# Kernel optimization log

Hardware: AMD Instinct MI355X
Metric: run time of the kernel (lower is better)

## Reference

```python
import jax, jax.numpy as jnp
import numpy as np

SEQ, BATCH, HIDDEN = 4096, 16, 512

def setup_inputs() -> dict:
    key = jax.random.key(0)
    kf, kx, kh = jax.random.split(key, 3)
    f = jax.random.uniform(kf, (SEQ, BATCH, HIDDEN), dtype=jnp.float32)
    x = jax.random.normal(kx, (SEQ, BATCH, HIDDEN), dtype=jnp.float32)
    hidden_init = jax.random.normal(kh, (BATCH, HIDDEN), dtype=jnp.float32)
    return {"f": f, "x": x, "hidden_init": hidden_init}

def reference(f, x, hidden_init):
    # h_t = f_t * x_t + (1 - f_t) * h_{t-1}
    # Linear recurrence h_t = a_t * h_{t-1} + b_t with a = 1-f, b = f*x.
    # Solved with an associative scan: compose (a1,b1) then (a2,b2) ->
    # (a1*a2, a2*b1 + b2). After the scan, A_t = prod(a_1..a_t) and
    # B_t = h_t assuming h_0 = 0, so h_t = B_t + A_t * h_init.
    a = 1.0 - f                      # (S, B, H)
    b = f * x                        # (S, B, H)

    def combine(c1, c2):
        a1, b1 = c1
        a2, b2 = c2
        return (a1 * a2, a2 * b1 + b2)

    A, B = jax.lax.associative_scan(combine, (a, b), axis=0)
    return B + A * hidden_init[None, :, :]
```

## Files before the change

kernel.cpp:

```cpp
#include <hip/hip_runtime.h>


#define SQ      4096
#define NC4     2048
#define NCH     8192
#define TT      16
#define NCHUNK  (SQ / TT)
#define GRID1   (NCHUNK * 8)

typedef float floatx4 __attribute__((ext_vector_type(4)));

__global__ __launch_bounds__(256, 2)
void fm_agg(const floatx4* __restrict__ f4, const floatx4* __restrict__ x4,
            floatx4* __restrict__ aggA, floatx4* __restrict__ aggB)
{
  const int tid   = threadIdx.x;
  const int chunk = blockIdx.x >> 3;
  const int col   = ((blockIdx.x & 7) << 8) + tid;
  const size_t base = (size_t)(chunk * TT) * NC4 + col;

  floatx4 ff[TT], xx[TT];
#pragma unroll
  for (int t = 0; t < TT; ++t) {
    ff[t] = f4[base + (size_t)t * NC4];
    xx[t] = x4[base + (size_t)t * NC4];
  }
  __builtin_amdgcn_sched_barrier(0);

  floatx4 A = {1.f, 1.f, 1.f, 1.f};
  floatx4 B = {0.f, 0.f, 0.f, 0.f};
#pragma unroll
  for (int t = 0; t < TT; ++t) {
    B.x = fmaf(ff[t].x, xx[t].x - B.x, B.x);
    B.y = fmaf(ff[t].y, xx[t].y - B.y, B.y);
    B.z = fmaf(ff[t].z, xx[t].z - B.z, B.z);
    B.w = fmaf(ff[t].w, xx[t].w - B.w, B.w);
    A.x = fmaf(-ff[t].x, A.x, A.x);
    A.y = fmaf(-ff[t].y, A.y, A.y);
    A.z = fmaf(-ff[t].z, A.z, A.z);
    A.w = fmaf(-ff[t].w, A.w, A.w);
  }
  aggA[(size_t)chunk * NC4 + col] = A;
  aggB[(size_t)chunk * NC4 + col] = B;
}

__global__ __launch_bounds__(256, 4)
void fm_mid(const float* __restrict__ A, float* __restrict__ B,
            const float* __restrict__ h0)
{
  const int chain = blockIdx.x * 256 + threadIdx.x;
  float h = h0[chain];
  for (int cb = 0; cb < NCHUNK / 16; ++cb) {
    float a[16], b[16];
#pragma unroll
    for (int i = 0; i < 16; ++i) {
      const size_t idx = (size_t)(cb * 16 + i) * NCH + chain;
      a[i] = A[idx];
      b[i] = B[idx];
    }
#pragma unroll
    for (int i = 0; i < 16; ++i) {
      const size_t idx = (size_t)(cb * 16 + i) * NCH + chain;
      B[idx] = h;
      h = fmaf(a[i], h, b[i]);
    }
  }
}

__global__ __launch_bounds__(256, 2)
void fm_apply(const floatx4* __restrict__ f4, const floatx4* __restrict__ x4,
              const floatx4* __restrict__ hprev4, floatx4* __restrict__ out4)
{
  const int tid   = threadIdx.x;
  const int chunk = (NCHUNK - 1) - (blockIdx.x >> 3);
  const int col   = ((blockIdx.x & 7) << 8) + tid;
  const size_t base = (size_t)(chunk * TT) * NC4 + col;

  floatx4 ff[TT], xx[TT];
#pragma unroll
  for (int t = 0; t < TT; ++t) {
    ff[t] = f4[base + (size_t)t * NC4];
    xx[t] = x4[base + (size_t)t * NC4];
  }
  floatx4 h = hprev4[(size_t)chunk * NC4 + col];
  __builtin_amdgcn_sched_barrier(0);

#pragma unroll
  for (int t = 0; t < TT; ++t) {
    h.x = fmaf(ff[t].x, xx[t].x - h.x, h.x);
    h.y = fmaf(ff[t].y, xx[t].y - h.y, h.y);
    h.z = fmaf(ff[t].z, xx[t].z - h.z, h.z);
    h.w = fmaf(ff[t].w, xx[t].w - h.w, h.w);
    __builtin_nontemporal_store(h, &out4[base + (size_t)t * NC4]);
  }
}

__global__ void fm_naive(const float4* __restrict__ f4, const float4* __restrict__ x4,
                         const float4* __restrict__ h04, float4* __restrict__ out4)
{
  const int col = blockIdx.x * blockDim.x + threadIdx.x;
  if (col >= NC4) return;
  float4 h = h04[col];
  for (int t = 0; t < SQ; ++t) {
    const size_t idx = (size_t)t * NC4 + col;
    const float4 ff = f4[idx], xx = x4[idx];
    h.x = fmaf(ff.x, xx.x - h.x, h.x);
    h.y = fmaf(ff.y, xx.y - h.y, h.y);
    h.z = fmaf(ff.z, xx.z - h.z, h.z);
    h.w = fmaf(ff.w, xx.w - h.w, h.w);
    out4[idx] = h;
  }
}

extern "C" void kernel_launch(void* const* d_in, const int* in_sizes, int n_in,
                              void* d_out, int out_size, void* d_ws, size_t ws_size,
                              hipStream_t stream)
{
  const floatx4* f4  = (const floatx4*)d_in[0];
  const floatx4* x4  = (const floatx4*)d_in[1];
  const float*   h0  = (const float*)d_in[2];
  floatx4* out4 = (floatx4*)d_out;

  const size_t AGG = (size_t)NCHUNK * NC4 * 16;

  if (ws_size >= 2 * AGG) {
    floatx4* aggA = (floatx4*)d_ws;
    floatx4* aggB = (floatx4*)((char*)d_ws + AGG);
    fm_agg<<<GRID1, 256, 0, stream>>>(f4, x4, aggA, aggB);
    fm_mid<<<NCH / 256, 256, 0, stream>>>((const float*)aggA,
                                          (float*)aggB, h0);
    fm_apply<<<GRID1, 256, 0, stream>>>(f4, x4, (const floatx4*)aggB, out4);
  } else {
    fm_naive<<<(NC4 + 255) / 256, 256, 0, stream>>>((const float4*)f4,
                                                    (const float4*)x4,
                                                    (const float4*)h0,
                                                    (float4*)out4);
  }
}
```

Baseline: 371.0 us.

## Fuse three-pass scan into one cooperative kernel with grid barriers

Replaces the three separate launches (chunk aggregate, serial chunk-carry, apply) with a single cooperative kernel of 256 blocks that uses software grid barriers between phases. The middle carry pass is parallelised into a two-level scan over 16 segments, so the long serial chain over 256 chunks becomes short chains. Chunk length doubles to 32 and the fallback kernels stream loads instead of register-buffering them. This removes launch gaps and the single-chain latency bottleneck, at the cost of a barrier memset, spin-wait synchronisation and a dependence on cooperative-launch support and co-residency.

```diff
diff --git a/kernel.cpp b/kernel.cpp
--- a/kernel.cpp
+++ b/kernel.cpp
@@ -4,41 +4,171 @@
 #define SQ      4096
 #define NC4     2048
 #define NCH     8192
-#define TT      16
+#define TT      32
 #define NCHUNK  (SQ / TT)
-#define GRID1   (NCHUNK * 8)
+#define NBLK    256
+#define SEGS    16
+#define CPS     (NCHUNK / SEGS)
+
+#define AGGA_OFF  0u
+#define AGGB_OFF  4194304u
+#define SEGA_OFF  8388608u
+#define SEGB_OFF  8912896u
+#define SEGH_OFF  9437184u
+#define BAR_OFF   9961472u
+#define WS_NEED   (BAR_OFF + 2048u)
 
 typedef float floatx4 __attribute__((ext_vector_type(4)));
 
-__global__ __launch_bounds__(256, 2)
+#define FM_B(B,F,X) \
+  B.x = fmaf(F.x, X.x - B.x, B.x); B.y = fmaf(F.y, X.y - B.y, B.y); \
+  B.z = fmaf(F.z, X.z - B.z, B.z); B.w = fmaf(F.w, X.w - B.w, B.w);
+#define FM_A(A,F) \
+  A.x = fmaf(-F.x, A.x, A.x); A.y = fmaf(-F.y, A.y, A.y); \
+  A.z = fmaf(-F.z, A.z, A.z); A.w = fmaf(-F.w, A.w, A.w);
+
+__device__ __forceinline__ void grid_barrier(unsigned* bar, int gen)
+{
+  __syncthreads();
+  if (threadIdx.x == 0) {
+    __threadfence();
+    __hip_atomic_fetch_add(&bar[(gen * 8 + (blockIdx.x & 7)) * 16], 1u,
+                           __ATOMIC_RELEASE, __HIP_MEMORY_SCOPE_AGENT);
+    unsigned sum;
+    do {
+      sum = 0;
+#pragma unroll
+      for (int s = 0; s < 8; ++s)
+        sum += __hip_atomic_load(&bar[(gen * 8 + s) * 16],
+                                 __ATOMIC_RELAXED, __HIP_MEMORY_SCOPE_AGENT);
+      if (sum < (unsigned)NBLK) __builtin_amdgcn_s_sleep(8);
+    } while (sum < (unsigned)NBLK);
+    __threadfence();
+  }
+  __syncthreads();
+}
+
+__global__ __launch_bounds__(512, 2)
+void fm_fused(const floatx4* __restrict__ f4, const floatx4* __restrict__ x4,
+              const float* __restrict__ h0, char* __restrict__ ws,
+              floatx4* __restrict__ out4)
+{
+  floatx4*  aggA4 = (floatx4*)(ws + AGGA_OFF);
+  floatx4*  aggB4 = (floatx4*)(ws + AGGB_OFF);
+  float*    aggAs = (float*)(ws + AGGA_OFF);
+  float*    aggBs = (float*)(ws + AGGB_OFF);
+  float*    segA  = (float*)(ws + SEGA_OFF);
+  float*    segB  = (float*)(ws + SEGB_OFF);
+  float*    segH  = (float*)(ws + SEGH_OFF);
+  unsigned* bar   = (unsigned*)(ws + BAR_OFF);
+
+  const int bid = blockIdx.x, tid = threadIdx.x;
+  const int chunk = bid >> 1;
+  const int c0 = ((bid & 1) << 10) + tid;
+  const int c1 = c0 + 512;
+  const size_t tbase = (size_t)chunk * TT * NC4;
+
+  {
+    floatx4 A0 = {1.f,1.f,1.f,1.f}, A1 = {1.f,1.f,1.f,1.f};
+    floatx4 B0 = {0.f,0.f,0.f,0.f}, B1 = {0.f,0.f,0.f,0.f};
+#pragma unroll 8
+    for (int t = 0; t < TT; ++t) {
+      const size_t r = tbase + (size_t)t * NC4;
+      const floatx4 F0 = f4[r + c0], X0 = x4[r + c0];
+      const floatx4 F1 = f4[r + c1], X1 = x4[r + c1];
+      FM_B(B0, F0, X0)  FM_A(A0, F0)
+      FM_B(B1, F1, X1)  FM_A(A1, F1)
+    }
+    aggA4[(size_t)chunk * NC4 + c0] = A0;
+    aggA4[(size_t)chunk * NC4 + c1] = A1;
+    aggB4[(size_t)chunk * NC4 + c0] = B0;
+    aggB4[(size_t)chunk * NC4 + c1] = B1;
+  }
+  grid_barrier(bar, 0);
+
+  {
+    const int g = bid * 512 + tid;
+    const int chain = g & (NCH - 1);
+    const int seg   = g >> 13;
+    float a = 1.f, b = 0.f;
+#pragma unroll
+    for (int i = 0; i < CPS; ++i) {
+      const size_t idx = (size_t)(seg * CPS + i) * NCH + chain;
+      const float ac = aggAs[idx], bc = aggBs[idx];
+      b = fmaf(ac, b, bc);
+      a *= ac;
+    }
+    segA[seg * NCH + chain] = a;
+    segB[seg * NCH + chain] = b;
+  }
+  grid_barrier(bar, 1);
+
+  if (bid < 16) {
+    const int chain = bid * 512 + tid;
+    float h = h0[chain];
+#pragma unroll
+    for (int s = 0; s < SEGS; ++s) {
+      segH[s * NCH + chain] = h;
+      h = fmaf(segA[s * NCH + chain], h, segB[s * NCH + chain]);
+    }
+  }
+  grid_barrier(bar, 2);
+
+  {
+    const int g = bid * 512 + tid;
+    const int chain = g & (NCH - 1);
+    const int seg   = g >> 13;
+    float h = segH[seg * NCH + chain];
+    float a[CPS], b[CPS];
+#pragma unroll
+    for (int i = 0; i < CPS; ++i) {
+      const size_t idx = (size_t)(seg * CPS + i) * NCH + chain;
+      a[i] = aggAs[idx];
+      b[i] = aggBs[idx];
+    }
+#pragma unroll
+    for (int i = 0; i < CPS; ++i) {
+      const size_t idx = (size_t)(seg * CPS + i) * NCH + chain;
+      aggBs[idx] = h;
+      h = fmaf(a[i], h, b[i]);
+    }
+  }
+  grid_barrier(bar, 3);
+
+  {
+    floatx4 H0 = aggB4[(size_t)chunk * NC4 + c0];
+    floatx4 H1 = aggB4[(size_t)chunk * NC4 + c1];
+#pragma unroll 8
+    for (int t = 0; t < TT; ++t) {
+      const size_t r = tbase + (size_t)t * NC4;
+      const floatx4 F0 = f4[r + c0], X0 = x4[r + c0];
+      const floatx4 F1 = f4[r + c1], X1 = x4[r + c1];
+      FM_B(H0, F0, X0)
+      FM_B(H1, F1, X1)
+      __builtin_nontemporal_store(H0, &out4[r + c0]);
+      __builtin_nontemporal_store(H1, &out4[r + c1]);
+    }
+  }
+}
+
+#define FTT     16
+#define FNCHUNK (SQ / FTT)
+
+__global__ __launch_bounds__(256, 4)
 void fm_agg(const floatx4* __restrict__ f4, const floatx4* __restrict__ x4,
             floatx4* __restrict__ aggA, floatx4* __restrict__ aggB)
 {
   const int tid   = threadIdx.x;
   const int chunk = blockIdx.x >> 3;
   const int col   = ((blockIdx.x & 7) << 8) + tid;
-  const size_t base = (size_t)(chunk * TT) * NC4 + col;
-
-  floatx4 ff[TT], xx[TT];
-#pragma unroll
-  for (int t = 0; t < TT; ++t) {
-    ff[t] = f4[base + (size_t)t * NC4];
-    xx[t] = x4[base + (size_t)t * NC4];
-  }
-  __builtin_amdgcn_sched_barrier(0);
-
-  floatx4 A = {1.f, 1.f, 1.f, 1.f};
-  floatx4 B = {0.f, 0.f, 0.f, 0.f};
-#pragma unroll
-  for (int t = 0; t < TT; ++t) {
-    B.x = fmaf(ff[t].x, xx[t].x - B.x, B.x);
-    B.y = fmaf(ff[t].y, xx[t].y - B.y, B.y);
-    B.z = fmaf(ff[t].z, xx[t].z - B.z, B.z);
-    B.w = fmaf(ff[t].w, xx[t].w - B.w, B.w);
-    A.x = fmaf(-ff[t].x, A.x, A.x);
-    A.y = fmaf(-ff[t].y, A.y, A.y);
-    A.z = fmaf(-ff[t].z, A.z, A.z);
-    A.w = fmaf(-ff[t].w, A.w, A.w);
+  const size_t base = (size_t)(chunk * FTT) * NC4 + col;
+
+  floatx4 A = {1.f,1.f,1.f,1.f}, B = {0.f,0.f,0.f,0.f};
+#pragma unroll 8
+  for (int t = 0; t < FTT; ++t) {
+    const floatx4 F = f4[base + (size_t)t * NC4];
+    const floatx4 X = x4[base + (size_t)t * NC4];
+    FM_B(B, F, X)  FM_A(A, F)
   }
   aggA[(size_t)chunk * NC4 + col] = A;
   aggB[(size_t)chunk * NC4 + col] = B;
@@ -50,7 +180,7 @@
 {
   const int chain = blockIdx.x * 256 + threadIdx.x;
   float h = h0[chain];
-  for (int cb = 0; cb < NCHUNK / 16; ++cb) {
+  for (int cb = 0; cb < FNCHUNK / 16; ++cb) {
     float a[16], b[16];
 #pragma unroll
     for (int i = 0; i < 16; ++i) {
@@ -67,47 +197,35 @@
   }
 }
 
-__global__ __launch_bounds__(256, 2)
+__global__ __launch_bounds__(256, 4)
 void fm_apply(const floatx4* __restrict__ f4, const floatx4* __restrict__ x4,
               const floatx4* __restrict__ hprev4, floatx4* __restrict__ out4)
 {
   const int tid   = threadIdx.x;
-  const int chunk = (NCHUNK - 1) - (blockIdx.x >> 3);
+  const int chunk = (FNCHUNK - 1) - (blockIdx.x >> 3);
   const int col   = ((blockIdx.x & 7) << 8) + tid;
-  const size_t base = (size_t)(chunk * TT) * NC4 + col;
-
-  floatx4 ff[TT], xx[TT];
-#pragma unroll
-  for (int t = 0; t < TT; ++t) {
-    ff[t] = f4[base + (size_t)t * NC4];
-    xx[t] = x4[base + (size_t)t * NC4];
-  }
+  const size_t base = (size_t)(chunk * FTT) * NC4 + col;
+
   floatx4 h = hprev4[(size_t)chunk * NC4 + col];
-  __builtin_amdgcn_sched_barrier(0);
-
-#pragma unroll
-  for (int t = 0; t < TT; ++t) {
-    h.x = fmaf(ff[t].x, xx[t].x - h.x, h.x);
-    h.y = fmaf(ff[t].y, xx[t].y - h.y, h.y);
-    h.z = fmaf(ff[t].z, xx[t].z - h.z, h.z);
-    h.w = fmaf(ff[t].w, xx[t].w - h.w, h.w);
+#pragma unroll 8
+  for (int t = 0; t < FTT; ++t) {
+    const floatx4 F = f4[base + (size_t)t * NC4];
+    const floatx4 X = x4[base + (size_t)t * NC4];
+    FM_B(h, F, X)
     __builtin_nontemporal_store(h, &out4[base + (size_t)t * NC4]);
   }
 }
 
-__global__ void fm_naive(const float4* __restrict__ f4, const float4* __restrict__ x4,
-                         const float4* __restrict__ h04, float4* __restrict__ out4)
+__global__ void fm_naive(const floatx4* __restrict__ f4, const floatx4* __restrict__ x4,
+                         const floatx4* __restrict__ h04, floatx4* __restrict__ out4)
 {
   const int col = blockIdx.x * blockDim.x + threadIdx.x;
   if (col >= NC4) return;
-  float4 h = h04[col];
+  floatx4 h = h04[col];
   for (int t = 0; t < SQ; ++t) {
     const size_t idx = (size_t)t * NC4 + col;
-    const float4 ff = f4[idx], xx = x4[idx];
-    h.x = fmaf(ff.x, xx.x - h.x, h.x);
-    h.y = fmaf(ff.y, xx.y - h.y, h.y);
-    h.z = fmaf(ff.z, xx.z - h.z, h.z);
-    h.w = fmaf(ff.w, xx.w - h.w, h.w);
+    const floatx4 F = f4[idx], X = x4[idx];
+    FM_B(h, F, X)
     out4[idx] = h;
   }
 }
@@ -121,19 +239,47 @@
   const float*   h0  = (const float*)d_in[2];
   floatx4* out4 = (floatx4*)d_out;
 
-  const size_t AGG = (size_t)NCHUNK * NC4 * 16;
-
+  static int coopOK = -1;
+  if (coopOK < 0) {
+    int dev = 0;
+    hipGetDevice(&dev);
+    hipDeviceProp_t prop;
+    int blocksPerCU = 0;
+    if (hipGetDeviceProperties(&prop, dev) == hipSuccess &&
+        prop.cooperativeLaunch &&
+        hipOccupancyMaxActiveBlocksPerMultiprocessor(
+            &blocksPerCU, (const void*)fm_fused, 512, 0) == hipSuccess &&
+        blocksPerCU >= 1 &&
+        (long long)blocksPerCU * prop.multiProcessorCount >= NBLK) {
+      coopOK = 1;
+    } else {
+      coopOK = 0;
+    }
+  }
+
+  if (ws_size >= WS_NEED && coopOK == 1) {
+    char* ws = (char*)d_ws;
+    hipMemsetAsync(ws + BAR_OFF, 0, 2048, stream);
+    void* args[5];
+    args[0] = (void*)&f4; args[1] = (void*)&x4; args[2] = (void*)&h0;
+    args[3] = (void*)&ws; args[4] = (void*)&out4;
+    hipError_t e = hipLaunchCooperativeKernel((const void*)fm_fused,
+                                              dim3(NBLK), dim3(512),
+                                              args, 0, stream);
+    if (e == hipSuccess) return;
+    coopOK = 0;
+  }
+
+  const size_t AGG = (size_t)FNCHUNK * NC4 * 16;
   if (ws_size >= 2 * AGG) {
     floatx4* aggA = (floatx4*)d_ws;
     floatx4* aggB = (floatx4*)((char*)d_ws + AGG);
-    fm_agg<<<GRID1, 256, 0, stream>>>(f4, x4, aggA, aggB);
+    fm_agg<<<FNCHUNK * 8, 256, 0, stream>>>(f4, x4, aggA, aggB);
     fm_mid<<<NCH / 256, 256, 0, stream>>>((const float*)aggA,
                                           (float*)aggB, h0);
-    fm_apply<<<GRID1, 256, 0, stream>>>(f4, x4, (const floatx4*)aggB, out4);
+    fm_apply<<<FNCHUNK * 8, 256, 0, stream>>>(f4, x4, (const floatx4*)aggB, out4);
   } else {
-    fm_naive<<<(NC4 + 255) / 256, 256, 0, stream>>>((const float4*)f4,
-                                                    (const float4*)x4,
-                                                    (const float4*)h0,
-                                                    (float4*)out4);
-  }
-}
+    fm_naive<<<(NC4 + 255) / 256, 256, 0, stream>>>(f4, x4,
+                                                    (const floatx4*)h0, out4);
+  }
+}
```

Result: no change. 374.9 us (+1.1%).

## Use larger time chunks and stream loads instead of preloading all steps

Applied to the files above, without the earlier changes.

The time chunk per block grows from 16 to 64 steps, so there are four times fewer chunks. That shrinks the aggregate arrays and the sequential work in the middle scan by the same factor. The agg and apply kernels no longer preload every step into registers before a scheduling barrier; they stream loads in a loop unrolled by 8 and raise the occupancy hint to 4 blocks per CU. The trade is fewer blocks in the parallel phases and less explicit memory-level parallelism per thread, in exchange for less mid-phase traffic and lower register pressure.

```diff
diff --git a/kernel.cpp b/kernel.cpp
--- a/kernel.cpp
+++ b/kernel.cpp
@@ -4,13 +4,20 @@
 #define SQ      4096
 #define NC4     2048
 #define NCH     8192
-#define TT      16
+#define TT      64
 #define NCHUNK  (SQ / TT)
 #define GRID1   (NCHUNK * 8)
 
 typedef float floatx4 __attribute__((ext_vector_type(4)));
 
-__global__ __launch_bounds__(256, 2)
+#define FM_B(B,F,X) \
+  B.x = fmaf(F.x, X.x - B.x, B.x); B.y = fmaf(F.y, X.y - B.y, B.y); \
+  B.z = fmaf(F.z, X.z - B.z, B.z); B.w = fmaf(F.w, X.w - B.w, B.w);
+#define FM_A(A,F) \
+  A.x = fmaf(-F.x, A.x, A.x); A.y = fmaf(-F.y, A.y, A.y); \
+  A.z = fmaf(-F.z, A.z, A.z); A.w = fmaf(-F.w, A.w, A.w);
+
+__global__ __launch_bounds__(256, 4)
 void fm_agg(const floatx4* __restrict__ f4, const floatx4* __restrict__ x4,
             floatx4* __restrict__ aggA, floatx4* __restrict__ aggB)
 {
@@ -19,26 +26,12 @@
   const int col   = ((blockIdx.x & 7) << 8) + tid;
   const size_t base = (size_t)(chunk * TT) * NC4 + col;
 
-  floatx4 ff[TT], xx[TT];
-#pragma unroll
+  floatx4 A = {1.f,1.f,1.f,1.f}, B = {0.f,0.f,0.f,0.f};
+#pragma unroll 8
   for (int t = 0; t < TT; ++t) {
-    ff[t] = f4[base + (size_t)t * NC4];
-    xx[t] = x4[base + (size_t)t * NC4];
-  }
-  __builtin_amdgcn_sched_barrier(0);
-
-  floatx4 A = {1.f, 1.f, 1.f, 1.f};
-  floatx4 B = {0.f, 0.f, 0.f, 0.f};
-#pragma unroll
-  for (int t = 0; t < TT; ++t) {
-    B.x = fmaf(ff[t].x, xx[t].x - B.x, B.x);
-    B.y = fmaf(ff[t].y, xx[t].y - B.y, B.y);
-    B.z = fmaf(ff[t].z, xx[t].z - B.z, B.z);
-    B.w = fmaf(ff[t].w, xx[t].w - B.w, B.w);
-    A.x = fmaf(-ff[t].x, A.x, A.x);
-    A.y = fmaf(-ff[t].y, A.y, A.y);
-    A.z = fmaf(-ff[t].z, A.z, A.z);
-    A.w = fmaf(-ff[t].w, A.w, A.w);
+    const floatx4 F = f4[base + (size_t)t * NC4];
+    const floatx4 X = x4[base + (size_t)t * NC4];
+    FM_B(B, F, X)  FM_A(A, F)
   }
   aggA[(size_t)chunk * NC4 + col] = A;
   aggB[(size_t)chunk * NC4 + col] = B;
@@ -67,7 +60,7 @@
   }
 }
 
-__global__ __launch_bounds__(256, 2)
+__global__ __launch_bounds__(256, 4)
 void fm_apply(const floatx4* __restrict__ f4, const floatx4* __restrict__ x4,
               const floatx4* __restrict__ hprev4, floatx4* __restrict__ out4)
 {
@@ -76,38 +69,26 @@
   const int col   = ((blockIdx.x & 7) << 8) + tid;
   const size_t base = (size_t)(chunk * TT) * NC4 + col;
 
-  floatx4 ff[TT], xx[TT];
-#pragma unroll
+  floatx4 h = hprev4[(size_t)chunk * NC4 + col];
+#pragma unroll 8
   for (int t = 0; t < TT; ++t) {
-    ff[t] = f4[base + (size_t)t * NC4];
-    xx[t] = x4[base + (size_t)t * NC4];
-  }
-  floatx4 h = hprev4[(size_t)chunk * NC4 + col];
-  __builtin_amdgcn_sched_barrier(0);
-
-#pragma unroll
-  for (int t = 0; t < TT; ++t) {
-    h.x = fmaf(ff[t].x, xx[t].x - h.x, h.x);
-    h.y = fmaf(ff[t].y, xx[t].y - h.y, h.y);
-    h.z = fmaf(ff[t].z, xx[t].z - h.z, h.z);
-    h.w = fmaf(ff[t].w, xx[t].w - h.w, h.w);
+    const floatx4 F = f4[base + (size_t)t * NC4];
+    const floatx4 X = x4[base + (size_t)t * NC4];
+    FM_B(h, F, X)
     __builtin_nontemporal_store(h, &out4[base + (size_t)t * NC4]);
   }
 }
 
-__global__ void fm_naive(const float4* __restrict__ f4, const float4* __restrict__ x4,
-                         const float4* __restrict__ h04, float4* __restrict__ out4)
+__global__ void fm_naive(const floatx4* __restrict__ f4, const floatx4* __restrict__ x4,
+                         const floatx4* __restrict__ h04, floatx4* __restrict__ out4)
 {
   const int col = blockIdx.x * blockDim.x + threadIdx.x;
   if (col >= NC4) return;
-  float4 h = h04[col];
+  floatx4 h = h04[col];
   for (int t = 0; t < SQ; ++t) {
     const size_t idx = (size_t)t * NC4 + col;
-    const float4 ff = f4[idx], xx = x4[idx];
-    h.x = fmaf(ff.x, xx.x - h.x, h.x);
-    h.y = fmaf(ff.y, xx.y - h.y, h.y);
-    h.z = fmaf(ff.z, xx.z - h.z, h.z);
-    h.w = fmaf(ff.w, xx.w - h.w, h.w);
+    const floatx4 F = f4[idx], X = x4[idx];
+    FM_B(h, F, X)
     out4[idx] = h;
   }
 }
@@ -131,9 +112,7 @@
                                           (float*)aggB, h0);
     fm_apply<<<GRID1, 256, 0, stream>>>(f4, x4, (const floatx4*)aggB, out4);
   } else {
-    fm_naive<<<(NC4 + 255) / 256, 256, 0, stream>>>((const float4*)f4,
-                                                    (const float4*)x4,
-                                                    (const float4*)h0,
-                                                    (float4*)out4);
+    fm_naive<<<(NC4 + 255) / 256, 256, 0, stream>>>(f4, x4,
+                                                    (const floatx4*)h0, out4);
   }
 }
```

New measurement: 361.3 us. -2.6%, faster.
